# Optimization experiments

Measured on AMD Instinct MI355X. Metric: run time of the kernel, lower is better.

The kernel has to match this reference:

```python
import jax, jax.numpy as jnp
import numpy as np

B, T, D, H, W = 512, 4096, 8, 16, 16  # batch, timesteps, data_size, hidden_size, width_size


def lipswish(x):
    return 0.909 * jax.nn.silu(x)


def _linear_params(key, out_f, in_f):
    kw, kb = jax.random.split(key)
    lim = 1.0 / np.sqrt(in_f)
    w = jax.random.uniform(kw, (out_f, in_f), minval=-lim, maxval=lim, dtype=jnp.float32)
    b = jax.random.uniform(kb, (out_f,), minval=-lim, maxval=lim, dtype=jnp.float32)
    return w, b


def setup_inputs() -> dict:
    key = jax.random.key(0)
    ks = jax.random.split(key, 9)
    ts = jnp.arange(T, dtype=jnp.float32)
    ys = jax.random.normal(ks[0], (B, T, D), dtype=jnp.float32)
    # initial MLP: (D+1) -> W -> H, relu hidden, identity final
    iW1, ib1 = _linear_params(ks[1], W, D + 1)
    iW2, ib2 = _linear_params(ks[2], H, W)
    # vf MLP: (H+1) -> W -> H, lipswish hidden, tanh final; scale=False -> ones (identity)
    vW1, vb1 = _linear_params(ks[3], W, H + 1)
    vW2, vb2 = _linear_params(ks[4], H, W)
    # cvf MLP: (H+1) -> W -> H*D, lipswish hidden, tanh final; scale=False -> ones
    cW1, cb1 = _linear_params(ks[5], W, H + 1)
    cW2, cb2 = _linear_params(ks[6], H * D, W)
    # readout: H -> 1
    rW, rb = _linear_params(ks[7], 1, H)
    return dict(ts=ts, ys=ys, iW1=iW1, ib1=ib1, iW2=iW2, ib2=ib2,
                vW1=vW1, vb1=vb1, vW2=vW2, vb2=vb2,
                cW1=cW1, cb1=cb1, cW2=cW2, cb2=cb2, rW=rW, rb=rb)


def reference(ts, ys, iW1, ib1, iW2, ib2, vW1, vb1, vW2, vb2,
              cW1, cb1, cW2, cb2, rW, rb):
    Bn, Tn, Dn = ys.shape
    Hn = iW2.shape[0]
    # initial hidden state: initial MLP on concat([t0, y0])
    init_in = jnp.concatenate([jnp.broadcast_to(ts[0], (Bn, 1)), ys[:, 0]], axis=1)  # (B, D+1)
    y0 = jax.nn.relu(init_in @ iW1.T + ib1) @ iW2.T + ib2  # (B, H)
    # Euler with dt=1 on integer-spaced ts: control increment = ys[n+1]-ys[n]
    dX = jnp.swapaxes(ys[:, 1:] - ys[:, :-1], 0, 1)  # (T-1, B, D)
    t_steps = ts[0] + jnp.arange(Tn - 1, dtype=ys.dtype)  # (T-1,)

    def step(y, inp):
        t, dx = inp  # scalar, (B, D)
        z = jnp.concatenate([jnp.broadcast_to(t, (Bn, 1)), y], axis=1)  # (B, H+1)
        f = jnp.tanh(lipswish(z @ vW1.T + vb1) @ vW2.T + vb2)           # (B, H) drift
        g = jnp.tanh(lipswish(z @ cW1.T + cb1) @ cW2.T + cb2)           # (B, H*D)
        g = g.reshape(Bn, Hn, Dn)
        y = y + f + jnp.einsum('bhd,bd->bh', g, dx)  # dt = 1.0
        return y, None

    yT, _ = jax.lax.scan(step, y0, (t_steps, dX))
    saved = jnp.stack([y0, yT], axis=1)  # SaveAt(t0=True, t1=True) -> (B, 2, H)
    return saved @ rW.T + rb  # (B, 2, 1)
```

## Files before the change

### kernel.cpp

```cpp
#include <hip/hip_runtime.h>

#define T_LEN 4096

typedef float v2f __attribute__((ext_vector_type(2)));

__device__ __forceinline__ float frcp(float x) { return __builtin_amdgcn_rcpf(x); }
__device__ __forceinline__ float fexp2(float x) { return __builtin_amdgcn_exp2f(x); }

__device__ __forceinline__ float rl(float v, int lane) {
  return __int_as_float(__builtin_amdgcn_readlane(__float_as_int(v), lane));
}
__device__ __forceinline__ float rfl(float v) {
  return __int_as_float(__builtin_amdgcn_readfirstlane(__float_as_int(v)));
}

__device__ __forceinline__ void pk_fma_s(v2f& acc, v2f w, v2f s) {
  asm("v_pk_fma_f32 %0, %1, %2, %0" : "+v"(acc) : "v"(w), "s"(s));
}

template <int CTRL>
__device__ __forceinline__ float dpp_add(float x) {
  int t = __builtin_amdgcn_mov_dpp(__float_as_int(x), CTRL, 0xF, 0xF, true);
  return x + __int_as_float(t);
}

__global__ __launch_bounds__(64) void disc_kernel(
    const float* __restrict__ ts, const float* __restrict__ ys,
    const float* __restrict__ iW1, const float* __restrict__ ib1,
    const float* __restrict__ iW2, const float* __restrict__ ib2,
    const float* __restrict__ vW1, const float* __restrict__ vb1,
    const float* __restrict__ vW2, const float* __restrict__ vb2,
    const float* __restrict__ cW1, const float* __restrict__ cb1,
    const float* __restrict__ cW2, const float* __restrict__ cb2,
    const float* __restrict__ rW, const float* __restrict__ rb,
    float* __restrict__ out)
{
  const int b   = blockIdx.x;
  const int l   = threadIdx.x;
  const int h16 = l & 15;
  const int p   = (l >> 4) & 1;
  const int hf  = l >> 2;
  const int d0  = (2 * l) & 7;

  __shared__ __align__(16) float sbuf[16];
  __shared__ __align__(16) float ybuf[16];
  __shared__ __align__(16) float xbuf[1024];

  const float* __restrict__ ysb = ys + (size_t)b * (T_LEN * 8);

  const float NL2E = -1.4426950408889634f;
  const float TSW  = 2.0f * 1.4426950408889634f * 0.909f;
  const float TSB  = 2.0f * 1.4426950408889634f;
  const float NLN2 = -0.6931471805599453f;

  float w1t, b1m;
  v2f W1y2[8];
  {
    const float* W1 = p ? cW1 : vW1;
    const float* bv = p ? cb1 : vb1;
    w1t = NL2E * W1[h16 * 17];
    b1m = NL2E * bv[h16];
#pragma unroll
    for (int k = 0; k < 8; ++k) {
      v2f w; w.x = NL2E * W1[h16 * 17 + 1 + 2 * k];
             w.y = NL2E * W1[h16 * 17 + 2 + 2 * k];
      W1y2[k] = w;
    }
  }
  v2f W2p[8], G0p[8], G1p[8];
#pragma unroll
  for (int k = 0; k < 8; ++k) {
    v2f a; a.x = TSW * vW2[hf * 16 + 2 * k]; a.y = TSW * vW2[hf * 16 + 2 * k + 1];
    W2p[k] = a;
    v2f c0; c0.x = TSW * cW2[(2 * l) * 16 + 2 * k]; c0.y = TSW * cW2[(2 * l) * 16 + 2 * k + 1];
    G0p[k] = c0;
    v2f c1; c1.x = TSW * cW2[(2 * l + 1) * 16 + 2 * k]; c1.y = TSW * cW2[(2 * l + 1) * 16 + 2 * k + 1];
    G1p[k] = c1;
  }
  const float b2p  = TSB * vb2[hf];
  const float bg0p = TSB * cb2[2 * l];
  const float bg1p = TSB * cb2[2 * l + 1];

  const float t0 = ts[0];

  float y_own;
  v2f yu2[8];
  {
    float acc = ib1[h16] + iW1[h16 * 9] * t0;
#pragma unroll
    for (int d = 0; d < 8; ++d) acc = fmaf(iW1[h16 * 9 + 1 + d], ysb[d], acc);
    acc = fmaxf(acc, 0.0f);
    sbuf[h16] = acc;
    float acc2 = ib2[h16];
#pragma unroll
    for (int k = 0; k < 16; ++k) acc2 = fmaf(iW2[h16 * 16 + k], sbuf[k], acc2);
    ybuf[h16] = acc2;
    y_own = ybuf[hf];
#pragma unroll
    for (int k = 0; k < 8; ++k) {
      v2f r; r.x = rfl(ybuf[2 * k]); r.y = rfl(ybuf[2 * k + 1]);
      yu2[k] = r;
    }
  }

  {
    float o = rb[0];
#pragma unroll
    for (int k = 0; k < 8; ++k) {
      o = fmaf(rW[2 * k], yu2[k].x, o);
      o = fmaf(rW[2 * k + 1], yu2[k].y, o);
    }
    if (l == 0) out[2 * b] = o;
  }

  const int CLAMP = T_LEN * 8 - 4;
  float4 A, Bq, Cq, Dq;
  {
    const int f0 = l * 8;
    A  = *(const float4*)(ysb + min(f0,      CLAMP));
    Bq = *(const float4*)(ysb + min(f0 + 4,  CLAMP));
    Cq = *(const float4*)(ysb + min(f0 + 8,  CLAMP));
    Dq = *(const float4*)(ysb + min(f0 + 12, CLAMP));
    float4 e0, e1;
    e0.x = Cq.x - A.x;  e0.y = Cq.y - A.y;  e0.z = Cq.z - A.z;  e0.w = Cq.w - A.w;
    e1.x = Dq.x - Bq.x; e1.y = Dq.y - Bq.y; e1.z = Dq.z - Bq.z; e1.w = Dq.w - Bq.w;
    *(float4*)(xbuf + l * 8)     = e0;
    *(float4*)(xbuf + l * 8 + 4) = e1;
  }

  float t = t0;
  for (int c = 0; c < 64; ++c) {
    {
      const int cn = min(c + 1, 63);
      const int f0 = cn * 512 + l * 8;
      A  = *(const float4*)(ysb + min(f0,      CLAMP));
      Bq = *(const float4*)(ysb + min(f0 + 4,  CLAMP));
      Cq = *(const float4*)(ysb + min(f0 + 8,  CLAMP));
      Dq = *(const float4*)(ysb + min(f0 + 12, CLAMP));
    }
    const float* __restrict__ xb = xbuf + (c & 1) * 512;
    const int base = c * 64;
    const int nsteps = min(64, (T_LEN - 1) - base);
    for (int j = 0; j < nsteps; ++j) {
      const v2f dx = *(const v2f*)(xb + j * 8 + d0);

      const float m_t = fmaf(w1t, t, b1m);
      v2f ma; ma.x = m_t; ma.y = 0.0f;
      v2f mb; mb.x = 0.0f; mb.y = 0.0f;
#pragma unroll
      for (int k = 0; k < 4; ++k) {
        pk_fma_s(ma, W1y2[k], yu2[k]);
        pk_fma_s(mb, W1y2[4 + k], yu2[4 + k]);
      }
      const v2f ms = ma + mb;
      const float m = ms.x + ms.y;
      const float eM = fexp2(m);
      const float u  = m * NLN2;
      const float s  = u * frcp(1.0f + eM);

      v2f su2[16];
#pragma unroll
      for (int k = 8; k < 16; ++k) {
        v2f r; r.x = rl(s, 2 * k); r.y = rl(s, 2 * k + 1);
        su2[k] = r;
      }
      v2f ga; ga.x = bg0p; ga.y = 0.0f;
      v2f gc; gc.x = 0.0f; gc.y = 0.0f;
      v2f gb; gb.x = bg1p; gb.y = 0.0f;
      v2f gd; gd.x = 0.0f; gd.y = 0.0f;
#pragma unroll
      for (int k = 0; k < 4; ++k) {
        pk_fma_s(ga, G0p[k],     su2[8 + k]);
        pk_fma_s(gc, G0p[4 + k], su2[12 + k]);
        pk_fma_s(gb, G1p[k],     su2[8 + k]);
        pk_fma_s(gd, G1p[4 + k], su2[12 + k]);
      }
#pragma unroll
      for (int k = 0; k < 8; ++k) {
        v2f r; r.x = rl(s, 2 * k); r.y = rl(s, 2 * k + 1);
        su2[k] = r;
      }
      v2f fa; fa.x = b2p; fa.y = 0.0f;
      v2f fb; fb.x = 0.0f; fb.y = 0.0f;
#pragma unroll
      for (int k = 0; k < 4; ++k) {
        pk_fma_s(fa, W2p[k],     su2[k]);
        pk_fma_s(fb, W2p[4 + k], su2[4 + k]);
      }

      const v2f gs0 = ga + gc;
      const v2f gs1 = gb + gd;
      const float g0v = fmaf(-2.0f, frcp(1.0f + fexp2(gs0.x + gs0.y)), 1.0f);
      const float g1v = fmaf(-2.0f, frcp(1.0f + fexp2(gs1.x + gs1.y)), 1.0f);
      const v2f fs = fa + fb;
      const float fv = fmaf(-2.0f, frcp(1.0f + fexp2(fs.x + fs.y)), 1.0f);

      float pr = fmaf(g0v, dx.x, g1v * dx.y);
      pr = dpp_add<0xB1>(pr);
      pr = dpp_add<0x4E>(pr);

      y_own = y_own + (fv + pr);
#pragma unroll
      for (int k = 0; k < 8; ++k) {
        v2f r; r.x = rl(y_own, 8 * k); r.y = rl(y_own, 8 * k + 4);
        yu2[k] = r;
      }
      t += 1.0f;
    }
    float* xbn = xbuf + ((c + 1) & 1) * 512;
    float4 e0, e1;
    e0.x = Cq.x - A.x;  e0.y = Cq.y - A.y;  e0.z = Cq.z - A.z;  e0.w = Cq.w - A.w;
    e1.x = Dq.x - Bq.x; e1.y = Dq.y - Bq.y; e1.z = Dq.z - Bq.z; e1.w = Dq.w - Bq.w;
    *(float4*)(xbn + l * 8)     = e0;
    *(float4*)(xbn + l * 8 + 4) = e1;
  }

  {
    float o = rb[0];
#pragma unroll
    for (int k = 0; k < 8; ++k) {
      o = fmaf(rW[2 * k], yu2[k].x, o);
      o = fmaf(rW[2 * k + 1], yu2[k].y, o);
    }
    if (l == 0) out[2 * b + 1] = o;
  }
}

extern "C" void kernel_launch(void* const* d_in, const int* in_sizes, int n_in,
                              void* d_out, int out_size, void* d_ws, size_t ws_size,
                              hipStream_t stream) {
  (void)in_sizes; (void)n_in; (void)out_size; (void)d_ws; (void)ws_size;
  const float* ts  = (const float*)d_in[0];
  const float* ys  = (const float*)d_in[1];
  const float* iW1 = (const float*)d_in[2];
  const float* ib1 = (const float*)d_in[3];
  const float* iW2 = (const float*)d_in[4];
  const float* ib2 = (const float*)d_in[5];
  const float* vW1 = (const float*)d_in[6];
  const float* vb1 = (const float*)d_in[7];
  const float* vW2 = (const float*)d_in[8];
  const float* vb2 = (const float*)d_in[9];
  const float* cW1 = (const float*)d_in[10];
  const float* cb1 = (const float*)d_in[11];
  const float* cW2 = (const float*)d_in[12];
  const float* cb2 = (const float*)d_in[13];
  const float* rW  = (const float*)d_in[14];
  const float* rb  = (const float*)d_in[15];
  float* out = (float*)d_out;
  hipLaunchKernelGGL(disc_kernel, dim3(512), dim3(64), 0, stream,
                     ts, ys, iW1, ib1, iW2, ib2, vW1, vb1, vW2, vb2,
                     cW1, cb1, cW2, cb2, rW, rb, out);
}
```

Before: 1.223 ms.

## Interleave two independent batch recurrences per wavefront for instruction-level parallelism

```diff
diff --git a/kernel.cpp b/kernel.cpp
--- a/kernel.cpp
+++ b/kernel.cpp
@@ -24,7 +24,96 @@
   return x + __int_as_float(t);
 }
 
-__global__ __launch_bounds__(64) void disc_kernel(
+#define NLN2f (-0.6931471805599453f)
+
+
+__device__ __forceinline__ float layer1_silu(float m_t, const v2f* W1y2,
+                                             const v2f* yu2) {
+  v2f ma; ma.x = m_t;  ma.y = 0.0f;
+  v2f mb; mb.x = 0.0f; mb.y = 0.0f;
+#pragma unroll
+  for (int k = 0; k < 4; ++k) {
+    pk_fma_s(ma, W1y2[k],     yu2[k]);
+    pk_fma_s(mb, W1y2[4 + k], yu2[4 + k]);
+  }
+  const v2f ms = ma + mb;
+  const float m = ms.x + ms.y;
+  const float eM = fexp2(m);
+  return (m * NLN2f) * frcp(1.0f + eM);
+}
+
+__device__ __forceinline__ void g_dots(float s, const v2f* G0p, const v2f* G1p,
+                                       float bg0p, float bg1p,
+                                       v2f& gs0, v2f& gs1) {
+  v2f su[8];
+#pragma unroll
+  for (int k = 0; k < 8; ++k) {
+    v2f r; r.x = rl(s, 16 + 2 * k); r.y = rl(s, 17 + 2 * k);
+    su[k] = r;
+  }
+  v2f ga; ga.x = bg0p; ga.y = 0.0f;
+  v2f gc; gc.x = 0.0f; gc.y = 0.0f;
+  v2f gb; gb.x = bg1p; gb.y = 0.0f;
+  v2f gd; gd.x = 0.0f; gd.y = 0.0f;
+#pragma unroll
+  for (int k = 0; k < 4; ++k) {
+    pk_fma_s(ga, G0p[k],     su[k]);
+    pk_fma_s(gc, G0p[4 + k], su[4 + k]);
+    pk_fma_s(gb, G1p[k],     su[k]);
+    pk_fma_s(gd, G1p[4 + k], su[4 + k]);
+  }
+  gs0 = ga + gc;
+  gs1 = gb + gd;
+}
+
+__device__ __forceinline__ v2f f_dots(float s, const v2f* W2p, float b2p) {
+  v2f su[8];
+#pragma unroll
+  for (int k = 0; k < 8; ++k) {
+    v2f r; r.x = rl(s, 2 * k); r.y = rl(s, 2 * k + 1);
+    su[k] = r;
+  }
+  v2f fa; fa.x = b2p;  fa.y = 0.0f;
+  v2f fb; fb.x = 0.0f; fb.y = 0.0f;
+#pragma unroll
+  for (int k = 0; k < 4; ++k) {
+    pk_fma_s(fa, W2p[k],     su[k]);
+    pk_fma_s(fb, W2p[4 + k], su[4 + k]);
+  }
+  return fa + fb;
+}
+
+__device__ __forceinline__ float finish_step(v2f gs0, v2f gs1, v2f fs, v2f dx,
+                                             float y_own) {
+  const float g0v = fmaf(-2.0f, frcp(1.0f + fexp2(gs0.x + gs0.y)), 1.0f);
+  const float g1v = fmaf(-2.0f, frcp(1.0f + fexp2(gs1.x + gs1.y)), 1.0f);
+  const float fv  = fmaf(-2.0f, frcp(1.0f + fexp2(fs.x + fs.y)), 1.0f);
+  float pr = fmaf(g0v, dx.x, g1v * dx.y);
+  pr = dpp_add<0xB1>(pr);
+  pr = dpp_add<0x4E>(pr);
+  return y_own + (fv + pr);
+}
+
+__device__ __forceinline__ void y_bcast(float yn, v2f* yu2) {
+#pragma unroll
+  for (int k = 0; k < 8; ++k) {
+    v2f r; r.x = rl(yn, 8 * k); r.y = rl(yn, 8 * k + 4);
+    yu2[k] = r;
+  }
+}
+
+__device__ __forceinline__ float readout(const float* __restrict__ rW,
+                                         float rb0, const v2f* yu2) {
+  float o = rb0;
+#pragma unroll
+  for (int k = 0; k < 8; ++k) {
+    o = fmaf(rW[2 * k],     yu2[k].x, o);
+    o = fmaf(rW[2 * k + 1], yu2[k].y, o);
+  }
+  return o;
+}
+
+__global__ __launch_bounds__(64, 1) void disc_kernel(
     const float* __restrict__ ts, const float* __restrict__ ys,
     const float* __restrict__ iW1, const float* __restrict__ ib1,
     const float* __restrict__ iW2, const float* __restrict__ ib2,
@@ -35,23 +124,26 @@
     const float* __restrict__ rW, const float* __restrict__ rb,
     float* __restrict__ out)
 {
-  const int b   = blockIdx.x;
+  const int b0  = blockIdx.x * 2;
   const int l   = threadIdx.x;
   const int h16 = l & 15;
   const int p   = (l >> 4) & 1;
   const int hf  = l >> 2;
   const int d0  = (2 * l) & 7;
 
-  __shared__ __align__(16) float sbuf[16];
-  __shared__ __align__(16) float ybuf[16];
-  __shared__ __align__(16) float xbuf[1024];
-
-  const float* __restrict__ ysb = ys + (size_t)b * (T_LEN * 8);
+  __shared__ __align__(16) float sbuf0[16];
+  __shared__ __align__(16) float sbuf1[16];
+  __shared__ __align__(16) float ybuf0[16];
+  __shared__ __align__(16) float ybuf1[16];
+  __shared__ __align__(16) float xbuf0[1024];
+  __shared__ __align__(16) float xbuf1[1024];
+
+  const float* __restrict__ ysb0 = ys + (size_t)b0 * (T_LEN * 8);
+  const float* __restrict__ ysb1 = ysb0 + (size_t)(T_LEN * 8);
 
   const float NL2E = -1.4426950408889634f;
   const float TSW  = 2.0f * 1.4426950408889634f * 0.909f;
   const float TSB  = 2.0f * 1.4426950408889634f;
-  const float NLN2 = -0.6931471805599453f;
 
   float w1t, b1m;
   v2f W1y2[8];
@@ -83,49 +175,70 @@
 
   const float t0 = ts[0];
 
-  float y_own;
-  v2f yu2[8];
+  float y_own0, y_own1;
+  v2f yu20[8], yu21[8];
   {
     float acc = ib1[h16] + iW1[h16 * 9] * t0;
 #pragma unroll
-    for (int d = 0; d < 8; ++d) acc = fmaf(iW1[h16 * 9 + 1 + d], ysb[d], acc);
-    acc = fmaxf(acc, 0.0f);
-    sbuf[h16] = acc;
+    for (int d = 0; d < 8; ++d) acc = fmaf(iW1[h16 * 9 + 1 + d], ysb0[d], acc);
+    sbuf0[h16] = fmaxf(acc, 0.0f);
+    float accB = ib1[h16] + iW1[h16 * 9] * t0;
+#pragma unroll
+    for (int d = 0; d < 8; ++d) accB = fmaf(iW1[h16 * 9 + 1 + d], ysb1[d], accB);
+    sbuf1[h16] = fmaxf(accB, 0.0f);
+
     float acc2 = ib2[h16];
-#pragma unroll
-    for (int k = 0; k < 16; ++k) acc2 = fmaf(iW2[h16 * 16 + k], sbuf[k], acc2);
-    ybuf[h16] = acc2;
-    y_own = ybuf[hf];
+    float acc3 = ib2[h16];
+#pragma unroll
+    for (int k = 0; k < 16; ++k) {
+      const float w = iW2[h16 * 16 + k];
+      acc2 = fmaf(w, sbuf0[k], acc2);
+      acc3 = fmaf(w, sbuf1[k], acc3);
+    }
+    ybuf0[h16] = acc2;
+    ybuf1[h16] = acc3;
+    y_own0 = ybuf0[hf];
+    y_own1 = ybuf1[hf];
 #pragma unroll
     for (int k = 0; k < 8; ++k) {
-      v2f r; r.x = rfl(ybuf[2 * k]); r.y = rfl(ybuf[2 * k + 1]);
-      yu2[k] = r;
-    }
-  }
-
-  {
-    float o = rb[0];
-#pragma unroll
-    for (int k = 0; k < 8; ++k) {
-      o = fmaf(rW[2 * k], yu2[k].x, o);
-      o = fmaf(rW[2 * k + 1], yu2[k].y, o);
-    }
-    if (l == 0) out[2 * b] = o;
+      v2f r0; r0.x = rfl(ybuf0[2 * k]); r0.y = rfl(ybuf0[2 * k + 1]);
+      yu20[k] = r0;
+      v2f r1; r1.x = rfl(ybuf1[2 * k]); r1.y = rfl(ybuf1[2 * k + 1]);
+      yu21[k] = r1;
+    }
+  }
+
+  {
+    const float rb0 = rb[0];
+    const float o0 = readout(rW, rb0, yu20);
+    const float o1 = readout(rW, rb0, yu21);
+    if (l == 0) {
+      out[2 * b0]     = o0;
+      out[2 * b0 + 2] = o1;
+    }
   }
 
   const int CLAMP = T_LEN * 8 - 4;
-  float4 A, Bq, Cq, Dq;
+  float4 A0, B0, C0, D0, A1, B1, C1, D1;
   {
     const int f0 = l * 8;
-    A  = *(const float4*)(ysb + min(f0,      CLAMP));
-    Bq = *(const float4*)(ysb + min(f0 + 4,  CLAMP));
-    Cq = *(const float4*)(ysb + min(f0 + 8,  CLAMP));
-    Dq = *(const float4*)(ysb + min(f0 + 12, CLAMP));
+    A0 = *(const float4*)(ysb0 + min(f0,      CLAMP));
+    B0 = *(const float4*)(ysb0 + min(f0 + 4,  CLAMP));
+    C0 = *(const float4*)(ysb0 + min(f0 + 8,  CLAMP));
+    D0 = *(const float4*)(ysb0 + min(f0 + 12, CLAMP));
+    A1 = *(const float4*)(ysb1 + min(f0,      CLAMP));
+    B1 = *(const float4*)(ysb1 + min(f0 + 4,  CLAMP));
+    C1 = *(const float4*)(ysb1 + min(f0 + 8,  CLAMP));
+    D1 = *(const float4*)(ysb1 + min(f0 + 12, CLAMP));
     float4 e0, e1;
-    e0.x = Cq.x - A.x;  e0.y = Cq.y - A.y;  e0.z = Cq.z - A.z;  e0.w = Cq.w - A.w;
-    e1.x = Dq.x - Bq.x; e1.y = Dq.y - Bq.y; e1.z = Dq.z - Bq.z; e1.w = Dq.w - Bq.w;
-    *(float4*)(xbuf + l * 8)     = e0;
-    *(float4*)(xbuf + l * 8 + 4) = e1;
+    e0.x = C0.x - A0.x; e0.y = C0.y - A0.y; e0.z = C0.z - A0.z; e0.w = C0.w - A0.w;
+    e1.x = D0.x - B0.x; e1.y = D0.y - B0.y; e1.z = D0.z - B0.z; e1.w = D0.w - B0.w;
+    *(float4*)(xbuf0 + l * 8)     = e0;
+    *(float4*)(xbuf0 + l * 8 + 4) = e1;
+    e0.x = C1.x - A1.x; e0.y = C1.y - A1.y; e0.z = C1.z - A1.z; e0.w = C1.w - A1.w;
+    e1.x = D1.x - B1.x; e1.y = D1.y - B1.y; e1.z = D1.z - B1.z; e1.w = D1.w - B1.w;
+    *(float4*)(xbuf1 + l * 8)     = e0;
+    *(float4*)(xbuf1 + l * 8 + 4) = e1;
   }
 
   float t = t0;
@@ -133,96 +246,63 @@
     {
       const int cn = min(c + 1, 63);
       const int f0 = cn * 512 + l * 8;
-      A  = *(const float4*)(ysb + min(f0,      CLAMP));
-      Bq = *(const float4*)(ysb + min(f0 + 4,  CLAMP));
-      Cq = *(const float4*)(ysb + min(f0 + 8,  CLAMP));
-      Dq = *(const float4*)(ysb + min(f0 + 12, CLAMP));
-    }
-    const float* __restrict__ xb = xbuf + (c & 1) * 512;
+      A0 = *(const float4*)(ysb0 + min(f0,      CLAMP));
+      B0 = *(const float4*)(ysb0 + min(f0 + 4,  CLAMP));
+      C0 = *(const float4*)(ysb0 + min(f0 + 8,  CLAMP));
+      D0 = *(const float4*)(ysb0 + min(f0 + 12, CLAMP));
+      A1 = *(const float4*)(ysb1 + min(f0,      CLAMP));
+      B1 = *(const float4*)(ysb1 + min(f0 + 4,  CLAMP));
+      C1 = *(const float4*)(ysb1 + min(f0 + 8,  CLAMP));
+      D1 = *(const float4*)(ysb1 + min(f0 + 12, CLAMP));
+    }
+    const float* __restrict__ xb0 = xbuf0 + (c & 1) * 512;
+    const float* __restrict__ xb1 = xbuf1 + (c & 1) * 512;
     const int base = c * 64;
     const int nsteps = min(64, (T_LEN - 1) - base);
     for (int j = 0; j < nsteps; ++j) {
-      const v2f dx = *(const v2f*)(xb + j * 8 + d0);
+      const v2f dx0 = *(const v2f*)(xb0 + j * 8 + d0);
+      const v2f dx1 = *(const v2f*)(xb1 + j * 8 + d0);
 
       const float m_t = fmaf(w1t, t, b1m);
-      v2f ma; ma.x = m_t; ma.y = 0.0f;
-      v2f mb; mb.x = 0.0f; mb.y = 0.0f;
-#pragma unroll
-      for (int k = 0; k < 4; ++k) {
-        pk_fma_s(ma, W1y2[k], yu2[k]);
-        pk_fma_s(mb, W1y2[4 + k], yu2[4 + k]);
-      }
-      const v2f ms = ma + mb;
-      const float m = ms.x + ms.y;
-      const float eM = fexp2(m);
-      const float u  = m * NLN2;
-      const float s  = u * frcp(1.0f + eM);
-
-      v2f su2[16];
-#pragma unroll
-      for (int k = 8; k < 16; ++k) {
-        v2f r; r.x = rl(s, 2 * k); r.y = rl(s, 2 * k + 1);
-        su2[k] = r;
-      }
-      v2f ga; ga.x = bg0p; ga.y = 0.0f;
-      v2f gc; gc.x = 0.0f; gc.y = 0.0f;
-      v2f gb; gb.x = bg1p; gb.y = 0.0f;
-      v2f gd; gd.x = 0.0f; gd.y = 0.0f;
-#pragma unroll
-      for (int k = 0; k < 4; ++k) {
-        pk_fma_s(ga, G0p[k],     su2[8 + k]);
-        pk_fma_s(gc, G0p[4 + k], su2[12 + k]);
-        pk_fma_s(gb, G1p[k],     su2[8 + k]);
-        pk_fma_s(gd, G1p[4 + k], su2[12 + k]);
-      }
-#pragma unroll
-      for (int k = 0; k < 8; ++k) {
-        v2f r; r.x = rl(s, 2 * k); r.y = rl(s, 2 * k + 1);
-        su2[k] = r;
-      }
-      v2f fa; fa.x = b2p; fa.y = 0.0f;
-      v2f fb; fb.x = 0.0f; fb.y = 0.0f;
-#pragma unroll
-      for (int k = 0; k < 4; ++k) {
-        pk_fma_s(fa, W2p[k],     su2[k]);
-        pk_fma_s(fb, W2p[4 + k], su2[4 + k]);
-      }
-
-      const v2f gs0 = ga + gc;
-      const v2f gs1 = gb + gd;
-      const float g0v = fmaf(-2.0f, frcp(1.0f + fexp2(gs0.x + gs0.y)), 1.0f);
-      const float g1v = fmaf(-2.0f, frcp(1.0f + fexp2(gs1.x + gs1.y)), 1.0f);
-      const v2f fs = fa + fb;
-      const float fv = fmaf(-2.0f, frcp(1.0f + fexp2(fs.x + fs.y)), 1.0f);
-
-      float pr = fmaf(g0v, dx.x, g1v * dx.y);
-      pr = dpp_add<0xB1>(pr);
-      pr = dpp_add<0x4E>(pr);
-
-      y_own = y_own + (fv + pr);
-#pragma unroll
-      for (int k = 0; k < 8; ++k) {
-        v2f r; r.x = rl(y_own, 8 * k); r.y = rl(y_own, 8 * k + 4);
-        yu2[k] = r;
-      }
+
+      const float s0 = layer1_silu(m_t, W1y2, yu20);
+      const float s1 = layer1_silu(m_t, W1y2, yu21);
+
+      v2f gs00, gs01; g_dots(s0, G0p, G1p, bg0p, bg1p, gs00, gs01);
+      v2f gs10, gs11; g_dots(s1, G0p, G1p, bg0p, bg1p, gs10, gs11);
+
+      const v2f fs0 = f_dots(s0, W2p, b2p);
+      const v2f fs1 = f_dots(s1, W2p, b2p);
+
+      y_own0 = finish_step(gs00, gs01, fs0, dx0, y_own0);
+      y_own1 = finish_step(gs10, gs11, fs1, dx1, y_own1);
+
+      y_bcast(y_own0, yu20);
+      y_bcast(y_own1, yu21);
+
       t += 1.0f;
     }
-    float* xbn = xbuf + ((c + 1) & 1) * 512;
+    float* xbn0 = xbuf0 + ((c + 1) & 1) * 512;
+    float* xbn1 = xbuf1 + ((c + 1) & 1) * 512;
     float4 e0, e1;
-    e0.x = Cq.x - A.x;  e0.y = Cq.y - A.y;  e0.z = Cq.z - A.z;  e0.w = Cq.w - A.w;
-    e1.x = Dq.x - Bq.x; e1.y = Dq.y - Bq.y; e1.z = Dq.z - Bq.z; e1.w = Dq.w - Bq.w;
-    *(float4*)(xbn + l * 8)     = e0;
-    *(float4*)(xbn + l * 8 + 4) = e1;
-  }
-
-  {
-    float o = rb[0];
-#pragma unroll
-    for (int k = 0; k < 8; ++k) {
-      o = fmaf(rW[2 * k], yu2[k].x, o);
-      o = fmaf(rW[2 * k + 1], yu2[k].y, o);
-    }
-    if (l == 0) out[2 * b + 1] = o;
+    e0.x = C0.x - A0.x; e0.y = C0.y - A0.y; e0.z = C0.z - A0.z; e0.w = C0.w - A0.w;
+    e1.x = D0.x - B0.x; e1.y = D0.y - B0.y; e1.z = D0.z - B0.z; e1.w = D0.w - B0.w;
+    *(float4*)(xbn0 + l * 8)     = e0;
+    *(float4*)(xbn0 + l * 8 + 4) = e1;
+    e0.x = C1.x - A1.x; e0.y = C1.y - A1.y; e0.z = C1.z - A1.z; e0.w = C1.w - A1.w;
+    e1.x = D1.x - B1.x; e1.y = D1.y - B1.y; e1.z = D1.z - B1.z; e1.w = D1.w - B1.w;
+    *(float4*)(xbn1 + l * 8)     = e0;
+    *(float4*)(xbn1 + l * 8 + 4) = e1;
+  }
+
+  {
+    const float rb0 = rb[0];
+    const float o0 = readout(rW, rb0, yu20);
+    const float o1 = readout(rW, rb0, yu21);
+    if (l == 0) {
+      out[2 * b0 + 1] = o0;
+      out[2 * b0 + 3] = o1;
+    }
   }
 }
 
@@ -247,7 +327,7 @@
   const float* rW  = (const float*)d_in[14];
   const float* rb  = (const float*)d_in[15];
   float* out = (float*)d_out;
-  hipLaunchKernelGGL(disc_kernel, dim3(512), dim3(64), 0, stream,
+  hipLaunchKernelGGL(disc_kernel, dim3(256), dim3(64), 0, stream,
                      ts, ys, iW1, ib1, iW2, ib2, vW1, vb1, vW2, vb2,
                      cW1, cb1, cW2, cb2, rW, rb, out);
 }
```

Result: slower. 2.176 ms (+78.0%).

## Broadcast hidden state and activations through LDS instead of readlane

Applied to the files above, without the earlier changes.

```diff
diff --git a/kernel.cpp b/kernel.cpp
--- a/kernel.cpp
+++ b/kernel.cpp
@@ -3,25 +3,42 @@
 #define T_LEN 4096
 
 typedef float v2f __attribute__((ext_vector_type(2)));
+typedef float v4f __attribute__((ext_vector_type(4)));
 
 __device__ __forceinline__ float frcp(float x) { return __builtin_amdgcn_rcpf(x); }
 __device__ __forceinline__ float fexp2(float x) { return __builtin_amdgcn_exp2f(x); }
 
-__device__ __forceinline__ float rl(float v, int lane) {
-  return __int_as_float(__builtin_amdgcn_readlane(__float_as_int(v), lane));
-}
-__device__ __forceinline__ float rfl(float v) {
-  return __int_as_float(__builtin_amdgcn_readfirstlane(__float_as_int(v)));
-}
-
-__device__ __forceinline__ void pk_fma_s(v2f& acc, v2f w, v2f s) {
-  asm("v_pk_fma_f32 %0, %1, %2, %0" : "+v"(acc) : "v"(w), "s"(s));
+__device__ __forceinline__ void pk_fma_v(v2f& acc, v2f w, v2f s) {
+  asm("v_pk_fma_f32 %0, %1, %2, %0" : "+v"(acc) : "v"(w), "v"(s));
 }
 
 template <int CTRL>
 __device__ __forceinline__ float dpp_add(float x) {
   int t = __builtin_amdgcn_mov_dpp(__float_as_int(x), CTRL, 0xF, 0xF, true);
   return x + __int_as_float(t);
+}
+
+__device__ __forceinline__ void cfence() { asm volatile("" ::: "memory"); }
+
+#define NLN2f (-0.6931471805599453f)
+
+__device__ __forceinline__ float readout_lds(const float* cb,
+                                             const float* __restrict__ rW,
+                                             float rb0) {
+  v4f a = *(const v4f*)(cb + 64);
+  v4f b = *(const v4f*)(cb + 68);
+  v4f c = *(const v4f*)(cb + 72);
+  v4f d = *(const v4f*)(cb + 76);
+  float o = rb0;
+  o = fmaf(rW[0],  a.x, o); o = fmaf(rW[1],  a.y, o);
+  o = fmaf(rW[2],  a.z, o); o = fmaf(rW[3],  a.w, o);
+  o = fmaf(rW[4],  b.x, o); o = fmaf(rW[5],  b.y, o);
+  o = fmaf(rW[6],  b.z, o); o = fmaf(rW[7],  b.w, o);
+  o = fmaf(rW[8],  c.x, o); o = fmaf(rW[9],  c.y, o);
+  o = fmaf(rW[10], c.z, o); o = fmaf(rW[11], c.w, o);
+  o = fmaf(rW[12], d.x, o); o = fmaf(rW[13], d.y, o);
+  o = fmaf(rW[14], d.z, o); o = fmaf(rW[15], d.w, o);
+  return o;
 }
 
 __global__ __launch_bounds__(64) void disc_kernel(
@@ -41,9 +58,11 @@
   const int p   = (l >> 4) & 1;
   const int hf  = l >> 2;
   const int d0  = (2 * l) & 7;
+  const int q4  = 4 * (l & 3);
+  const int ywslot = ((l & 3) == 0) ? (64 + hf) : (80 + l);
 
   __shared__ __align__(16) float sbuf[16];
-  __shared__ __align__(16) float ybuf[16];
+  __shared__ __align__(16) float cbuf[160];
   __shared__ __align__(16) float xbuf[1024];
 
   const float* __restrict__ ysb = ys + (size_t)b * (T_LEN * 8);
@@ -51,7 +70,6 @@
   const float NL2E = -1.4426950408889634f;
   const float TSW  = 2.0f * 1.4426950408889634f * 0.909f;
   const float TSB  = 2.0f * 1.4426950408889634f;
-  const float NLN2 = -0.6931471805599453f;
 
   float w1t, b1m;
   v2f W1y2[8];
@@ -67,11 +85,16 @@
       W1y2[k] = w;
     }
   }
-  v2f W2p[8], G0p[8], G1p[8];
+  v2f W2q[2];
+#pragma unroll
+  for (int j = 0; j < 2; ++j) {
+    v2f w; w.x = TSW * vW2[hf * 16 + q4 + 2 * j];
+           w.y = TSW * vW2[hf * 16 + q4 + 2 * j + 1];
+    W2q[j] = w;
+  }
+  v2f G0p[8], G1p[8];
 #pragma unroll
   for (int k = 0; k < 8; ++k) {
-    v2f a; a.x = TSW * vW2[hf * 16 + 2 * k]; a.y = TSW * vW2[hf * 16 + 2 * k + 1];
-    W2p[k] = a;
     v2f c0; c0.x = TSW * cW2[(2 * l) * 16 + 2 * k]; c0.y = TSW * cW2[(2 * l) * 16 + 2 * k + 1];
     G0p[k] = c0;
     v2f c1; c1.x = TSW * cW2[(2 * l + 1) * 16 + 2 * k]; c1.y = TSW * cW2[(2 * l + 1) * 16 + 2 * k + 1];
@@ -84,32 +107,22 @@
   const float t0 = ts[0];
 
   float y_own;
-  v2f yu2[8];
   {
     float acc = ib1[h16] + iW1[h16 * 9] * t0;
 #pragma unroll
     for (int d = 0; d < 8; ++d) acc = fmaf(iW1[h16 * 9 + 1 + d], ysb[d], acc);
-    acc = fmaxf(acc, 0.0f);
-    sbuf[h16] = acc;
+    sbuf[h16] = fmaxf(acc, 0.0f);
+    cfence();
     float acc2 = ib2[h16];
 #pragma unroll
     for (int k = 0; k < 16; ++k) acc2 = fmaf(iW2[h16 * 16 + k], sbuf[k], acc2);
-    ybuf[h16] = acc2;
-    y_own = ybuf[hf];
-#pragma unroll
-    for (int k = 0; k < 8; ++k) {
-      v2f r; r.x = rfl(ybuf[2 * k]); r.y = rfl(ybuf[2 * k + 1]);
-      yu2[k] = r;
-    }
-  }
-
-  {
-    float o = rb[0];
-#pragma unroll
-    for (int k = 0; k < 8; ++k) {
-      o = fmaf(rW[2 * k], yu2[k].x, o);
-      o = fmaf(rW[2 * k + 1], yu2[k].y, o);
-    }
+    cbuf[64 + h16] = acc2;
+    cfence();
+    y_own = cbuf[64 + hf];
+  }
+
+  {
+    const float o = readout_lds(cbuf, rW, rb[0]);
     if (l == 0) out[2 * b] = o;
   }
 
@@ -126,6 +139,7 @@
     e1.x = Dq.x - Bq.x; e1.y = Dq.y - Bq.y; e1.z = Dq.z - Bq.z; e1.w = Dq.w - Bq.w;
     *(float4*)(xbuf + l * 8)     = e0;
     *(float4*)(xbuf + l * 8 + 4) = e1;
+    cfence();
   }
 
   float t = t0;
@@ -142,69 +156,71 @@
     const int base = c * 64;
     const int nsteps = min(64, (T_LEN - 1) - base);
     for (int j = 0; j < nsteps; ++j) {
+      const v4f ya = *(const v4f*)(cbuf + 64);
+      const v4f yb = *(const v4f*)(cbuf + 68);
+      const v4f yc = *(const v4f*)(cbuf + 72);
+      const v4f yd = *(const v4f*)(cbuf + 76);
       const v2f dx = *(const v2f*)(xb + j * 8 + d0);
 
       const float m_t = fmaf(w1t, t, b1m);
-      v2f ma; ma.x = m_t; ma.y = 0.0f;
+      v2f ma; ma.x = m_t;  ma.y = 0.0f;
       v2f mb; mb.x = 0.0f; mb.y = 0.0f;
-#pragma unroll
-      for (int k = 0; k < 4; ++k) {
-        pk_fma_s(ma, W1y2[k], yu2[k]);
-        pk_fma_s(mb, W1y2[4 + k], yu2[4 + k]);
-      }
+      pk_fma_v(ma, W1y2[0], ya.xy);
+      pk_fma_v(ma, W1y2[1], ya.zw);
+      pk_fma_v(ma, W1y2[2], yb.xy);
+      pk_fma_v(ma, W1y2[3], yb.zw);
+      pk_fma_v(mb, W1y2[4], yc.xy);
+      pk_fma_v(mb, W1y2[5], yc.zw);
+      pk_fma_v(mb, W1y2[6], yd.xy);
+      pk_fma_v(mb, W1y2[7], yd.zw);
       const v2f ms = ma + mb;
       const float m = ms.x + ms.y;
+
       const float eM = fexp2(m);
-      const float u  = m * NLN2;
-      const float s  = u * frcp(1.0f + eM);
-
-      v2f su2[16];
-#pragma unroll
-      for (int k = 8; k < 16; ++k) {
-        v2f r; r.x = rl(s, 2 * k); r.y = rl(s, 2 * k + 1);
-        su2[k] = r;
-      }
+      const float s  = (m * NLN2f) * frcp(1.0f + eM);
+
+      cbuf[l] = s;
+      cfence();
+      const v4f g0 = *(const v4f*)(cbuf + 16);
+      const v4f g1 = *(const v4f*)(cbuf + 20);
+      const v4f g2 = *(const v4f*)(cbuf + 24);
+      const v4f g3 = *(const v4f*)(cbuf + 28);
+      const v4f sf = *(const v4f*)(cbuf + q4);
+
       v2f ga; ga.x = bg0p; ga.y = 0.0f;
       v2f gc; gc.x = 0.0f; gc.y = 0.0f;
       v2f gb; gb.x = bg1p; gb.y = 0.0f;
       v2f gd; gd.x = 0.0f; gd.y = 0.0f;
-#pragma unroll
-      for (int k = 0; k < 4; ++k) {
-        pk_fma_s(ga, G0p[k],     su2[8 + k]);
-        pk_fma_s(gc, G0p[4 + k], su2[12 + k]);
-        pk_fma_s(gb, G1p[k],     su2[8 + k]);
-        pk_fma_s(gd, G1p[4 + k], su2[12 + k]);
-      }
-#pragma unroll
-      for (int k = 0; k < 8; ++k) {
-        v2f r; r.x = rl(s, 2 * k); r.y = rl(s, 2 * k + 1);
-        su2[k] = r;
-      }
-      v2f fa; fa.x = b2p; fa.y = 0.0f;
-      v2f fb; fb.x = 0.0f; fb.y = 0.0f;
-#pragma unroll
-      for (int k = 0; k < 4; ++k) {
-        pk_fma_s(fa, W2p[k],     su2[k]);
-        pk_fma_s(fb, W2p[4 + k], su2[4 + k]);
-      }
+      pk_fma_v(ga, G0p[0], g0.xy); pk_fma_v(ga, G0p[1], g0.zw);
+      pk_fma_v(ga, G0p[2], g1.xy); pk_fma_v(ga, G0p[3], g1.zw);
+      pk_fma_v(gc, G0p[4], g2.xy); pk_fma_v(gc, G0p[5], g2.zw);
+      pk_fma_v(gc, G0p[6], g3.xy); pk_fma_v(gc, G0p[7], g3.zw);
+      pk_fma_v(gb, G1p[0], g0.xy); pk_fma_v(gb, G1p[1], g0.zw);
+      pk_fma_v(gb, G1p[2], g1.xy); pk_fma_v(gb, G1p[3], g1.zw);
+      pk_fma_v(gd, G1p[4], g2.xy); pk_fma_v(gd, G1p[5], g2.zw);
+      pk_fma_v(gd, G1p[6], g3.xy); pk_fma_v(gd, G1p[7], g3.zw);
+
+      v2f fa; fa.x = 0.0f; fa.y = 0.0f;
+      pk_fma_v(fa, W2q[0], sf.xy);
+      pk_fma_v(fa, W2q[1], sf.zw);
+      float fp = fa.x + fa.y;
+      fp = dpp_add<0xB1>(fp);
+      fp = dpp_add<0x4E>(fp);
+      const float farg = fp + b2p;
 
       const v2f gs0 = ga + gc;
       const v2f gs1 = gb + gd;
       const float g0v = fmaf(-2.0f, frcp(1.0f + fexp2(gs0.x + gs0.y)), 1.0f);
       const float g1v = fmaf(-2.0f, frcp(1.0f + fexp2(gs1.x + gs1.y)), 1.0f);
-      const v2f fs = fa + fb;
-      const float fv = fmaf(-2.0f, frcp(1.0f + fexp2(fs.x + fs.y)), 1.0f);
+      const float fv  = fmaf(-2.0f, frcp(1.0f + fexp2(farg)), 1.0f);
 
       float pr = fmaf(g0v, dx.x, g1v * dx.y);
       pr = dpp_add<0xB1>(pr);
       pr = dpp_add<0x4E>(pr);
 
       y_own = y_own + (fv + pr);
-#pragma unroll
-      for (int k = 0; k < 8; ++k) {
-        v2f r; r.x = rl(y_own, 8 * k); r.y = rl(y_own, 8 * k + 4);
-        yu2[k] = r;
-      }
+      cbuf[ywslot] = y_own;
+      cfence();
       t += 1.0f;
     }
     float* xbn = xbuf + ((c + 1) & 1) * 512;
@@ -213,15 +229,11 @@
     e1.x = Dq.x - Bq.x; e1.y = Dq.y - Bq.y; e1.z = Dq.z - Bq.z; e1.w = Dq.w - Bq.w;
     *(float4*)(xbn + l * 8)     = e0;
     *(float4*)(xbn + l * 8 + 4) = e1;
-  }
-
-  {
-    float o = rb[0];
-#pragma unroll
-    for (int k = 0; k < 8; ++k) {
-      o = fmaf(rW[2 * k], yu2[k].x, o);
-      o = fmaf(rW[2 * k + 1], yu2[k].y, o);
-    }
+    cfence();
+  }
+
+  {
+    const float o = readout_lds(cbuf, rW, rb[0]);
     if (l == 0) out[2 * b + 1] = o;
   }
 }
```

Result: faster. 1.195 ms (-2.3%).
